# Kernel optimization log

Hardware: AMD Instinct MI355X
Metric: run time of the kernel (lower is better)

Reference implementation:

```python
import jax, jax.numpy as jnp
import numpy as np

B, L, K, D = 4, 48, 32, 128
EPS = 1e-5


def setup_inputs() -> dict:
    key = jax.random.key(0)
    ks = jax.random.split(key, 12)
    s = 1.0 / np.sqrt(D)
    s2 = 1.0 / np.sqrt(2 * D)
    return {
        "h": jax.random.normal(ks[0], (B, L, K, D), jnp.float32),
        # message_mlp: Linear(D,D) -> ReLU -> Linear(D,D); weights stored (in,out)
        "Wm1": jax.random.normal(ks[1], (D, D), jnp.float32) * s,
        "bm1": jnp.zeros((D,), jnp.float32),
        "Wm2": jax.random.normal(ks[2], (D, D), jnp.float32) * s,
        "bm2": jnp.zeros((D,), jnp.float32),
        # attn_mlp: Linear(2D,D) -> ReLU -> Linear(D,1)
        "Wa1": jax.random.normal(ks[3], (2 * D, D), jnp.float32) * s2,
        "ba1": jnp.zeros((D,), jnp.float32),
        "Wa2": jax.random.normal(ks[4], (D, 1), jnp.float32) * s,
        "ba2": jnp.zeros((1,), jnp.float32),
        # LayerNorm(D)
        "gamma": jnp.ones((D,), jnp.float32),
        "beta": jnp.zeros((D,), jnp.float32),
    }


def reference(h, Wm1, bm1, Wm2, bm2, Wa1, ba1, Wa2, ba2, gamma, beta):
    # messages: (B,L,K,D)
    messages = jax.nn.relu(h @ Wm1 + bm1) @ Wm2 + bm2

    # attn_mlp first layer on cat(h_i, h_j): split Wa1 so we never build the 2D concat
    hi_proj = h @ Wa1[:D]   # (B,L,K,D) contribution from h_i (varies over dim 1)
    hj_proj = h @ Wa1[D:]   # (B,L,K,D) contribution from h_j (varies over dim 2)
    # hidden: (B,L,L,K,D)
    hidden = jax.nn.relu(hi_proj[:, :, None, :, :] + hj_proj[:, None, :, :, :] + ba1)
    # logits: (B,L,L,K)
    attn_logits = jnp.einsum("bijkd,d->bijk", hidden, Wa2[:, 0]) + ba2[0]
    attn_weights = jax.nn.softmax(attn_logits, axis=2)  # softmax over j

    # aggregated[b,i,k,:] = sum_j w[b,i,j,k] * messages[b,j,k,:]
    aggregated = jnp.einsum("bijk,bjkd->bikd", attn_weights, messages)

    x = h + aggregated
    mu = jnp.mean(x, axis=-1, keepdims=True)
    var = jnp.mean(jnp.square(x - mu), axis=-1, keepdims=True)
    return (x - mu) * jax.lax.rsqrt(var + EPS) * gamma + beta
```

## Files before the change

### kernel.cpp

```cpp
#include <hip/hip_runtime.h>
#include <math.h>

#define Bc 4
#define Lc 48
#define Kc 32
#define Dc 128
#define ROWS (Bc*Lc*Kc)
#define RT 24
#define NRT (ROWS/RT)

static_assert(NRT == 256, "sel decode assumes 256 row tiles");

__device__ __forceinline__ void tile_gemm_body(
    const float* __restrict__ in, const float* __restrict__ W,
    const float* __restrict__ bias, float* __restrict__ out,
    int r0, bool relu)
{
    __shared__ float sA[RT*Dc];
    __shared__ float sB[Dc*Dc];
    __shared__ float sBias[Dc];
    const int tid = threadIdx.x;

    {
        const float4* src = (const float4*)W;
        float4* dst = (float4*)sB;
        #pragma unroll
        for (int i = 0; i < (Dc*Dc/4)/256; ++i) dst[tid + i*256] = src[tid + i*256];
    }
    {
        const float4* src = (const float4*)(in + r0*Dc);
        float4* dst = (float4*)sA;
        #pragma unroll
        for (int i = 0; i < (RT*Dc/4)/256; ++i) dst[tid + i*256] = src[tid + i*256];
    }
    if (tid < Dc/4) {
        float4 b4 = bias ? ((const float4*)bias)[tid] : make_float4(0.f,0.f,0.f,0.f);
        ((float4*)sBias)[tid] = b4;
    }
    __syncthreads();

    const int rg = tid >> 5;
    const int c0 = (tid & 31) * 4;
    const float* A0 = sA + rg*3*Dc;
    float acc[3][4] = {};

    #pragma unroll 8
    for (int k = 0; k < Dc; k += 4) {
        float4 a0 = *(const float4*)(A0 + k);
        float4 a1 = *(const float4*)(A0 + Dc + k);
        float4 a2 = *(const float4*)(A0 + 2*Dc + k);
        float4 b0 = *(const float4*)(sB + (k+0)*Dc + c0);
        float4 b1 = *(const float4*)(sB + (k+1)*Dc + c0);
        float4 b2 = *(const float4*)(sB + (k+2)*Dc + c0);
        float4 b3 = *(const float4*)(sB + (k+3)*Dc + c0);
        float a_[3][4] = {{a0.x,a0.y,a0.z,a0.w},{a1.x,a1.y,a1.z,a1.w},{a2.x,a2.y,a2.z,a2.w}};
        float b_[4][4] = {{b0.x,b0.y,b0.z,b0.w},{b1.x,b1.y,b1.z,b1.w},
                          {b2.x,b2.y,b2.z,b2.w},{b3.x,b3.y,b3.z,b3.w}};
        #pragma unroll
        for (int r = 0; r < 3; ++r)
            #pragma unroll
            for (int c = 0; c < 4; ++c)
                #pragma unroll
                for (int q = 0; q < 4; ++q)
                    acc[r][c] = fmaf(a_[r][q], b_[q][c], acc[r][c]);
    }

    #pragma unroll
    for (int r = 0; r < 3; ++r) {
        float4 v;
        v.x = acc[r][0] + sBias[c0+0];
        v.y = acc[r][1] + sBias[c0+1];
        v.z = acc[r][2] + sBias[c0+2];
        v.w = acc[r][3] + sBias[c0+3];
        if (relu) {
            v.x = fmaxf(v.x, 0.f); v.y = fmaxf(v.y, 0.f);
            v.z = fmaxf(v.z, 0.f); v.w = fmaxf(v.w, 0.f);
        }
        *(float4*)(out + (r0 + rg*3 + r)*Dc + c0) = v;
    }
}

__global__ __launch_bounds__(256) void k_gemm_t(
    const float* __restrict__ h, const float* __restrict__ Wm1,
    const float* __restrict__ bm1, float* __restrict__ t_ws)
{
    tile_gemm_body(h, Wm1, bm1, t_ws, blockIdx.x * RT, true);
}

__global__ __launch_bounds__(256) void k_gemm_rest(
    const float* __restrict__ h, const float* __restrict__ t_ws,
    const float* __restrict__ Wm2, const float* __restrict__ bm2,
    const float* __restrict__ Wa1, const float* __restrict__ ba1,
    float* __restrict__ msg_ws, float* __restrict__ hip_ws,
    float* __restrict__ hjp_ws)
{
    const int sel = blockIdx.x >> 8;
    const int r0  = (blockIdx.x & 255) * RT;
    const float* in; const float* W; const float* bias; float* out;
    if (sel == 0)      { in = t_ws; W = Wm2;          bias = bm2;     out = msg_ws; }
    else if (sel == 1) { in = h;    W = Wa1;          bias = ba1;     out = hip_ws; }
    else               { in = h;    W = Wa1 + Dc*Dc;  bias = nullptr; out = hjp_ws; }
    tile_gemm_body(in, W, bias, out, r0, false);
}

__global__ __launch_bounds__(512) void k_attn(
    const float* __restrict__ h,
    const float* __restrict__ hip_ws, const float* __restrict__ hjp_ws,
    const float* __restrict__ msg_ws,
    const float* __restrict__ wa2, const float* __restrict__ gamma,
    const float* __restrict__ beta, float* __restrict__ out)
{
    const int blk = blockIdx.x;
    const int b  = blk >> 6;
    const int k  = (blk >> 1) & 31;
    const int i0 = (blk & 1) * 24;

    __shared__ float HJ[48*132];
    __shared__ float MS[48*132];
    __shared__ float HI[24*132];
    __shared__ float WA[Dc];
    __shared__ float GM[Dc];
    __shared__ float BT[Dc];
    __shared__ float WT[24*48];

    const int tid = threadIdx.x;

    for (int idx = tid; idx < 48*32; idx += 512) {
        const int j = idx >> 5, c4 = (idx & 31) * 4;
        const int g = ((b*Lc + j)*Kc + k)*Dc + c4;
        *(float4*)(HJ + j*132 + c4) = *(const float4*)(hjp_ws + g);
        *(float4*)(MS + j*132 + c4) = *(const float4*)(msg_ws + g);
    }
    for (int idx = tid; idx < 24*32; idx += 512) {
        const int i = idx >> 5, c4 = (idx & 31) * 4;
        const int g = ((b*Lc + i0 + i)*Kc + k)*Dc + c4;
        *(float4*)(HI + i*132 + c4) = *(const float4*)(hip_ws + g);
    }
    if (tid < 32)       ((float4*)WA)[tid]      = ((const float4*)wa2)[tid];
    else if (tid < 64)  ((float4*)GM)[tid - 32] = ((const float4*)gamma)[tid - 32];
    else if (tid < 96)  ((float4*)BT)[tid - 64] = ((const float4*)beta)[tid - 64];
    __syncthreads();

    const int wave = tid >> 6;
    const int lane = tid & 63;
    const int il0  = wave * 3;
    const bool jv  = lane < 48;
    const int  jl  = jv ? lane : 0;

    float s0 = 0.f, s1 = 0.f, s2 = 0.f;
    {
        const float* hj = HJ + jl*132;
        const float* hA = HI + il0*132;
        const float* hB = hA + 132;
        const float* hC = hB + 132;
        #pragma unroll 4
        for (int d = 0; d < Dc; d += 4) {
            const float4 hj4 = *(const float4*)(hj + d);
            const float4 w4  = *(const float4*)(WA + d);
            const float4 a4  = *(const float4*)(hA + d);
            const float4 b4  = *(const float4*)(hB + d);
            const float4 c4  = *(const float4*)(hC + d);
            s0 = fmaf(fmaxf(a4.x + hj4.x, 0.f), w4.x, s0);
            s0 = fmaf(fmaxf(a4.y + hj4.y, 0.f), w4.y, s0);
            s0 = fmaf(fmaxf(a4.z + hj4.z, 0.f), w4.z, s0);
            s0 = fmaf(fmaxf(a4.w + hj4.w, 0.f), w4.w, s0);
            s1 = fmaf(fmaxf(b4.x + hj4.x, 0.f), w4.x, s1);
            s1 = fmaf(fmaxf(b4.y + hj4.y, 0.f), w4.y, s1);
            s1 = fmaf(fmaxf(b4.z + hj4.z, 0.f), w4.z, s1);
            s1 = fmaf(fmaxf(b4.w + hj4.w, 0.f), w4.w, s1);
            s2 = fmaf(fmaxf(c4.x + hj4.x, 0.f), w4.x, s2);
            s2 = fmaf(fmaxf(c4.y + hj4.y, 0.f), w4.y, s2);
            s2 = fmaf(fmaxf(c4.z + hj4.z, 0.f), w4.z, s2);
            s2 = fmaf(fmaxf(c4.w + hj4.w, 0.f), w4.w, s2);
        }
    }

    float sv[3] = { jv ? s0 : -1e30f, jv ? s1 : -1e30f, jv ? s2 : -1e30f };
    #pragma unroll
    for (int q = 0; q < 3; ++q) {
        float m = sv[q];
        #pragma unroll
        for (int off = 32; off; off >>= 1) m = fmaxf(m, __shfl_xor(m, off));
        const float p = jv ? __expf(sv[q] - m) : 0.f;
        float sum = p;
        #pragma unroll
        for (int off = 32; off; off >>= 1) sum += __shfl_xor(sum, off);
        if (jv) WT[(il0 + q)*48 + lane] = p / sum;
    }
    __syncthreads();

    const int d0 = lane * 2;
    float ac[3][2] = {};
    const float* wt0 = WT + il0*48;
    const float* wt1 = wt0 + 48;
    const float* wt2 = wt1 + 48;
    #pragma unroll 4
    for (int j = 0; j < 48; ++j) {
        const float2 m2 = *(const float2*)(MS + j*132 + d0);
        const float wA = wt0[j], wB = wt1[j], wC = wt2[j];
        ac[0][0] = fmaf(wA, m2.x, ac[0][0]); ac[0][1] = fmaf(wA, m2.y, ac[0][1]);
        ac[1][0] = fmaf(wB, m2.x, ac[1][0]); ac[1][1] = fmaf(wB, m2.y, ac[1][1]);
        ac[2][0] = fmaf(wC, m2.x, ac[2][0]); ac[2][1] = fmaf(wC, m2.y, ac[2][1]);
    }
    const float gm0 = GM[d0], gm1 = GM[d0+1], bt0 = BT[d0], bt1 = BT[d0+1];
    #pragma unroll
    for (int q = 0; q < 3; ++q) {
        const int i = i0 + il0 + q;
        const int g = ((b*Lc + i)*Kc + k)*Dc + d0;
        const float2 h2 = *(const float2*)(h + g);
        const float x0 = h2.x + ac[q][0];
        const float x1 = h2.y + ac[q][1];
        float ps = x0 + x1;
        float pq = x0*x0 + x1*x1;
        #pragma unroll
        for (int off = 32; off; off >>= 1) {
            ps += __shfl_xor(ps, off);
            pq += __shfl_xor(pq, off);
        }
        const float mu  = ps * (1.f/128.f);
        const float var = pq * (1.f/128.f) - mu*mu;
        const float rs  = rsqrtf(var + 1e-5f);
        float2 o2;
        o2.x = (x0 - mu)*rs*gm0 + bt0;
        o2.y = (x1 - mu)*rs*gm1 + bt1;
        *(float2*)(out + g) = o2;
    }
}

extern "C" void kernel_launch(void* const* d_in, const int* in_sizes, int n_in,
                              void* d_out, int out_size, void* d_ws, size_t ws_size,
                              hipStream_t stream)
{
    const float* h     = (const float*)d_in[0];
    const float* Wm1   = (const float*)d_in[1];
    const float* bm1   = (const float*)d_in[2];
    const float* Wm2   = (const float*)d_in[3];
    const float* bm2   = (const float*)d_in[4];
    const float* Wa1   = (const float*)d_in[5];
    const float* ba1   = (const float*)d_in[6];
    const float* wa2   = (const float*)d_in[7];
    const float* gamma = (const float*)d_in[9];
    const float* beta  = (const float*)d_in[10];

    float* t_ws   = (float*)d_ws;
    float* msg_ws = t_ws   + ROWS*Dc;
    float* hip_ws = msg_ws + ROWS*Dc;
    float* hjp_ws = hip_ws + ROWS*Dc;
    float* outp   = (float*)d_out;

    hipLaunchKernelGGL(k_gemm_t,    dim3(NRT),    dim3(256), 0, stream,
                       h, Wm1, bm1, t_ws);
    hipLaunchKernelGGL(k_gemm_rest, dim3(NRT*3),  dim3(256), 0, stream,
                       h, t_ws, Wm2, bm2, Wa1, ba1, msg_ws, hip_ws, hjp_ws);
    hipLaunchKernelGGL(k_attn,      dim3(Bc*Kc*2), dim3(512), 0, stream,
                       h, hip_ws, hjp_ws, msg_ws, wa2, gamma, beta, outp);
}
```

Before: 108.2 us.

## Fuse message MLP layers and projection GEMMs into a single kernel launch

Merges the two GEMM kernels into one launch. Blocks for the message path compute relu(h@Wm1+b) into shared memory and immediately apply Wm2, removing the intermediate global workspace round trip and one launch. The row tile grows from 24 to 48 with 512 threads per block, which halves the number of blocks and reloads each weight matrix less often. The cost is imbalanced work: message-role blocks do two GEMMs while projection blocks do one, and the larger shared memory footprint (about 114KB) limits blocks per CU.

```diff
diff --git a/kernel.cpp b/kernel.cpp
--- a/kernel.cpp
+++ b/kernel.cpp
@@ -6,44 +6,17 @@
 #define Kc 32
 #define Dc 128
 #define ROWS (Bc*Lc*Kc)
-#define RT 24
+#define RT 48
 #define NRT (ROWS/RT)
-
-static_assert(NRT == 256, "sel decode assumes 256 row tiles");
-
-__device__ __forceinline__ void tile_gemm_body(
-    const float* __restrict__ in, const float* __restrict__ W,
-    const float* __restrict__ bias, float* __restrict__ out,
-    int r0, bool relu)
-{
-    __shared__ float sA[RT*Dc];
-    __shared__ float sB[Dc*Dc];
-    __shared__ float sBias[Dc];
-    const int tid = threadIdx.x;
-
-    {
-        const float4* src = (const float4*)W;
-        float4* dst = (float4*)sB;
-        #pragma unroll
-        for (int i = 0; i < (Dc*Dc/4)/256; ++i) dst[tid + i*256] = src[tid + i*256];
-    }
-    {
-        const float4* src = (const float4*)(in + r0*Dc);
-        float4* dst = (float4*)sA;
-        #pragma unroll
-        for (int i = 0; i < (RT*Dc/4)/256; ++i) dst[tid + i*256] = src[tid + i*256];
-    }
-    if (tid < Dc/4) {
-        float4 b4 = bias ? ((const float4*)bias)[tid] : make_float4(0.f,0.f,0.f,0.f);
-        ((float4*)sBias)[tid] = b4;
-    }
-    __syncthreads();
-
-    const int rg = tid >> 5;
-    const int c0 = (tid & 31) * 4;
+#define GT 512
+
+static_assert(NRT == 128, "role decode assumes 128 row tiles");
+
+__device__ __forceinline__ void gemm_regs(
+    const float* __restrict__ sA, const float* __restrict__ sB,
+    int rg, int c0, float acc[3][4])
+{
     const float* A0 = sA + rg*3*Dc;
-    float acc[3][4] = {};
-
     #pragma unroll 8
     for (int k = 0; k < Dc; k += 4) {
         float4 a0 = *(const float4*)(A0 + k);
@@ -64,43 +37,95 @@
                 for (int q = 0; q < 4; ++q)
                     acc[r][c] = fmaf(a_[r][q], b_[q][c], acc[r][c]);
     }
-
-    #pragma unroll
-    for (int r = 0; r < 3; ++r) {
-        float4 v;
-        v.x = acc[r][0] + sBias[c0+0];
-        v.y = acc[r][1] + sBias[c0+1];
-        v.z = acc[r][2] + sBias[c0+2];
-        v.w = acc[r][3] + sBias[c0+3];
-        if (relu) {
-            v.x = fmaxf(v.x, 0.f); v.y = fmaxf(v.y, 0.f);
-            v.z = fmaxf(v.z, 0.f); v.w = fmaxf(v.w, 0.f);
-        }
-        *(float4*)(out + (r0 + rg*3 + r)*Dc + c0) = v;
-    }
-}
-
-__global__ __launch_bounds__(256) void k_gemm_t(
-    const float* __restrict__ h, const float* __restrict__ Wm1,
-    const float* __restrict__ bm1, float* __restrict__ t_ws)
-{
-    tile_gemm_body(h, Wm1, bm1, t_ws, blockIdx.x * RT, true);
-}
-
-__global__ __launch_bounds__(256) void k_gemm_rest(
-    const float* __restrict__ h, const float* __restrict__ t_ws,
+}
+
+__global__ __launch_bounds__(GT) void k_gemm_all(
+    const float* __restrict__ h,
+    const float* __restrict__ Wm1, const float* __restrict__ bm1,
     const float* __restrict__ Wm2, const float* __restrict__ bm2,
     const float* __restrict__ Wa1, const float* __restrict__ ba1,
     float* __restrict__ msg_ws, float* __restrict__ hip_ws,
     float* __restrict__ hjp_ws)
 {
-    const int sel = blockIdx.x >> 8;
-    const int r0  = (blockIdx.x & 255) * RT;
-    const float* in; const float* W; const float* bias; float* out;
-    if (sel == 0)      { in = t_ws; W = Wm2;          bias = bm2;     out = msg_ws; }
-    else if (sel == 1) { in = h;    W = Wa1;          bias = ba1;     out = hip_ws; }
-    else               { in = h;    W = Wa1 + Dc*Dc;  bias = nullptr; out = hjp_ws; }
-    tile_gemm_body(in, W, bias, out, r0, false);
+    __shared__ float sA[RT*Dc];
+    __shared__ float sT[RT*Dc];
+    __shared__ float sB[Dc*Dc];
+    __shared__ float sBias[Dc];
+
+    const int tid = threadIdx.x;
+    const int sel = blockIdx.x >> 7;
+    const int r0  = (blockIdx.x & 127) * RT;
+
+    const float* W1; const float* b1;
+    if (sel == 0)      { W1 = Wm1;          b1 = bm1; }
+    else if (sel == 1) { W1 = Wa1;          b1 = ba1; }
+    else               { W1 = Wa1 + Dc*Dc;  b1 = nullptr; }
+
+    {
+        const float4* src = (const float4*)W1;
+        float4* dst = (float4*)sB;
+        #pragma unroll
+        for (int i = 0; i < (Dc*Dc/4)/GT; ++i) dst[tid + i*GT] = src[tid + i*GT];
+        const float4* asrc = (const float4*)(h + r0*Dc);
+        float4* adst = (float4*)sA;
+        #pragma unroll
+        for (int i = 0; i < (RT*Dc/4)/GT; ++i) adst[tid + i*GT] = asrc[tid + i*GT];
+        if (tid < Dc/4)
+            ((float4*)sBias)[tid] = b1 ? ((const float4*)b1)[tid]
+                                       : make_float4(0.f, 0.f, 0.f, 0.f);
+    }
+    __syncthreads();
+
+    const int rg = tid >> 5;
+    const int c0 = (tid & 31) * 4;
+    float acc[3][4] = {};
+    gemm_regs(sA, sB, rg, c0, acc);
+
+    if (sel != 0) {
+        float* out = (sel == 1) ? hip_ws : hjp_ws;
+        #pragma unroll
+        for (int r = 0; r < 3; ++r) {
+            float4 v;
+            v.x = acc[r][0] + sBias[c0+0];
+            v.y = acc[r][1] + sBias[c0+1];
+            v.z = acc[r][2] + sBias[c0+2];
+            v.w = acc[r][3] + sBias[c0+3];
+            *(float4*)(out + (r0 + rg*3 + r)*Dc + c0) = v;
+        }
+        return;
+    }
+
+    #pragma unroll
+    for (int r = 0; r < 3; ++r) {
+        float4 v;
+        v.x = fmaxf(acc[r][0] + sBias[c0+0], 0.f);
+        v.y = fmaxf(acc[r][1] + sBias[c0+1], 0.f);
+        v.z = fmaxf(acc[r][2] + sBias[c0+2], 0.f);
+        v.w = fmaxf(acc[r][3] + sBias[c0+3], 0.f);
+        *(float4*)(sT + (rg*3+r)*Dc + c0) = v;
+    }
+    __syncthreads();
+
+    {
+        const float4* src = (const float4*)Wm2;
+        float4* dst = (float4*)sB;
+        #pragma unroll
+        for (int i = 0; i < (Dc*Dc/4)/GT; ++i) dst[tid + i*GT] = src[tid + i*GT];
+        if (tid < Dc/4) ((float4*)sBias)[tid] = ((const float4*)bm2)[tid];
+    }
+    __syncthreads();
+
+    float acc2[3][4] = {};
+    gemm_regs(sT, sB, rg, c0, acc2);
+    #pragma unroll
+    for (int r = 0; r < 3; ++r) {
+        float4 v;
+        v.x = acc2[r][0] + sBias[c0+0];
+        v.y = acc2[r][1] + sBias[c0+1];
+        v.z = acc2[r][2] + sBias[c0+2];
+        v.w = acc2[r][3] + sBias[c0+3];
+        *(float4*)(msg_ws + (r0 + rg*3 + r)*Dc + c0) = v;
+    }
 }
 
 __global__ __launch_bounds__(512) void k_attn(
@@ -242,16 +267,13 @@
     const float* gamma = (const float*)d_in[9];
     const float* beta  = (const float*)d_in[10];
 
-    float* t_ws   = (float*)d_ws;
-    float* msg_ws = t_ws   + ROWS*Dc;
+    float* msg_ws = (float*)d_ws;
     float* hip_ws = msg_ws + ROWS*Dc;
     float* hjp_ws = hip_ws + ROWS*Dc;
     float* outp   = (float*)d_out;
 
-    hipLaunchKernelGGL(k_gemm_t,    dim3(NRT),    dim3(256), 0, stream,
-                       h, Wm1, bm1, t_ws);
-    hipLaunchKernelGGL(k_gemm_rest, dim3(NRT*3),  dim3(256), 0, stream,
-                       h, t_ws, Wm2, bm2, Wa1, ba1, msg_ws, hip_ws, hjp_ws);
-    hipLaunchKernelGGL(k_attn,      dim3(Bc*Kc*2), dim3(512), 0, stream,
+    hipLaunchKernelGGL(k_gemm_all, dim3(NRT*3),  dim3(GT),  0, stream,
+                       h, Wm1, bm1, Wm2, bm2, Wa1, ba1, msg_ws, hip_ws, hjp_ws);
+    hipLaunchKernelGGL(k_attn,     dim3(Bc*Kc*2), dim3(512), 0, stream,
                        h, hip_ws, hjp_ws, msg_ws, wa2, gamma, beta, outp);
 }
```

Result: faster. 102.4 us (-5.4%).
